# Optimization experiments

Measured on AMD Instinct MI355X. Metric: run time of the kernel, lower is better.

## Reference

```python
import jax, jax.numpy as jnp
import numpy as np


def setup_inputs() -> dict:
    key = jax.random.key(0)
    ks = jax.random.split(key, 10)
    B, S, I, Hy, H = 16, 4096, 256, 64, 512
    sc = 0.05
    return {
        "x": jax.random.normal(ks[0], (B, S, I), jnp.float32),
        "hidden": jax.random.normal(ks[1], (B, H), jnp.float32),
        "lin0_W": jax.random.normal(ks[2], (Hy, I), jnp.float32) * sc,
        "lin0_b": jax.random.normal(ks[3], (Hy,), jnp.float32) * sc,
        "sig0_W": jax.random.normal(ks[4], (Hy, I), jnp.float32) * sc,
        "sig0_b": jax.random.normal(ks[5], (Hy,), jnp.float32) * sc,
        "fch_W": jax.random.normal(ks[6], (H, Hy), jnp.float32) * sc,
        "fch_b": jax.random.normal(ks[7], (H,), jnp.float32) * sc,
        "fc2_W": jax.random.normal(ks[8], (H, I), jnp.float32) * sc,
        "fc2_b": jax.random.normal(ks[9], (H,), jnp.float32) * sc,
    }


def reference(x, hidden, lin0_W, lin0_b, sig0_W, sig0_b, fch_W, fch_b, fc2_W, fc2_b):
    # GLN sub-network (num_layers=1): relu(linear(x) * sigmoid(linear(x)))
    lin = jnp.einsum('bsi,hi->bsh', x, lin0_W) + lin0_b          # [B,S,Hy]
    gate = jax.nn.sigmoid(jnp.einsum('bsi,hi->bsh', x, sig0_W) + sig0_b)
    g = jax.nn.relu(lin * gate)                                   # [B,S,Hy]
    b = jnp.einsum('bsh,dh->bsd', g, fch_W) + fch_b               # [B,S,H]
    # multihead gating
    sig_alphas = jax.nn.sigmoid(jnp.einsum('bsi,di->bsd', x, fc2_W) + fc2_b)
    b = b * sig_alphas

    # sequential recurrence: h_t = relu(b_t + roll(h_{t-1}, 1, -1)); h_{-1} = hidden
    def step(h, b_t):
        h = jax.nn.relu(b_t + jnp.roll(h, 1, axis=-1))
        return h, h

    b_tmajor = jnp.swapaxes(b, 0, 1)  # [S,B,H]
    last, outs = jax.lax.scan(step, hidden, b_tmajor)
    outputs = jnp.swapaxes(outs, 0, 1)  # [B,S,H]
    return outputs, last
```

## Files before the change

kernel.cpp:

```cpp
#include <hip/hip_runtime.h>

typedef __attribute__((ext_vector_type(4))) float  f32x4;
typedef __attribute__((ext_vector_type(4))) short  s16x4;
typedef __attribute__((ext_vector_type(8))) short  s16x8;
typedef __bf16 bf16x8 __attribute__((ext_vector_type(8)));

#define NBATCH 16
#define SEQ    4096
#define KIN    256
#define HY     64
#define HOUT   512
#define NROWS  (NBATCH*SEQ)
#define LC     32
#define NC     (SEQ/LC)

#define GP(x) ((const __attribute__((address_space(1))) void*)(x))
#define LP(x) ((__attribute__((address_space(3))) void*)(x))

static __device__ __forceinline__ short f2bf(float f) {
  unsigned u = __float_as_uint(f);
  u = u + 0x7FFF + ((u >> 16) & 1);
  return (short)(u >> 16);
}
static __device__ __forceinline__ float bf2f(short h) {
  return __uint_as_float(((unsigned)(unsigned short)h) << 16);
}
static __device__ __forceinline__ f32x4 mfma16(bf16x8 a, bf16x8 b, f32x4 c) {
  return __builtin_amdgcn_mfma_f32_16x16x32_bf16(a, b, c, 0, 0, 0);
}
static __device__ __forceinline__ bf16x8 ldfrag(const short* p) {
  return *reinterpret_cast<const bf16x8*>(p);
}
static __device__ __forceinline__ float fsigmoid(float z) {
  return 1.f / (1.f + __expf(-z));
}

__global__ void prep_w(const float* __restrict__ lin0W, const float* __restrict__ sig0W,
                       const float* __restrict__ fchW,  const float* __restrict__ fc2W,
                       short* __restrict__ W1h, short* __restrict__ W2h,
                       short* __restrict__ Fh,  short* __restrict__ F2h) {
  int i = blockIdx.x * 256 + threadIdx.x;
  if (i < 16384) {
    W1h[i] = f2bf(lin0W[i]);
    W2h[i] = f2bf(sig0W[i]);
  } else if (i < 16384 + 32768) {
    Fh[i - 16384] = f2bf(fchW[i - 16384]);
  } else if (i < 16384 + 32768 + 131072) {
    F2h[i - 49152] = f2bf(fc2W[i - 49152]);
  }
}

__global__ __launch_bounds__(256) void gx(
    const float* __restrict__ x,
    const short* __restrict__ W1h, const short* __restrict__ W2h,
    const float* __restrict__ lin0b, const float* __restrict__ sig0b,
    short* __restrict__ Gh, short* __restrict__ xh) {
  __shared__ __align__(16) short smem[64 * 256 + 64 * 64];
  short* Ah = smem;
  short* gL = smem + 64 * 256;
  int tid = threadIdx.x;
  int row0 = blockIdx.x * 64;
  #pragma unroll
  for (int i = 0; i < 8; ++i) {
    int slot = i * 256 + tid;
    int r = slot >> 5, k8 = slot & 31;
    const float* xp = x + (size_t)(row0 + r) * KIN + k8 * 8;
    f32x4 v0 = *reinterpret_cast<const f32x4*>(xp);
    f32x4 v1 = *reinterpret_cast<const f32x4*>(xp + 4);
    s16x8 hh;
    #pragma unroll
    for (int j = 0; j < 4; ++j) { hh[j] = f2bf(v0[j]); hh[4 + j] = f2bf(v1[j]); }
    *reinterpret_cast<s16x8*>(&Ah[(r * 256 + k8 * 8) ^ ((r & 7) << 3)]) = hh;
    *reinterpret_cast<s16x8*>(xh + (size_t)(row0 + r) * KIN + k8 * 8) = hh;
  }
  __syncthreads();
  int w = tid >> 6, l = tid & 63, lr = l & 15, lg = l >> 4;
  {
    int c = w * 16 + lr;
    f32x4 a1[4], a2[4];
    #pragma unroll
    for (int rt = 0; rt < 4; ++rt) { a1[rt] = (f32x4)0.f; a2[rt] = (f32x4)0.f; }
    #pragma unroll
    for (int ks = 0; ks < 8; ++ks) {
      int kk = ks * 32 + lg * 8;
      bf16x8 b1 = ldfrag(W1h + c * 256 + kk);
      bf16x8 b2 = ldfrag(W2h + c * 256 + kk);
      #pragma unroll
      for (int rt = 0; rt < 4; ++rt) {
        int r = rt * 16 + lr;
        bf16x8 a = ldfrag(&Ah[(r * 256 + kk) ^ ((r & 7) << 3)]);
        a1[rt] = mfma16(b1, a, a1[rt]);
        a2[rt] = mfma16(b2, a, a2[rt]);
      }
    }
    f32x4 blv = *reinterpret_cast<const f32x4*>(lin0b + w * 16 + lg * 4);
    f32x4 bsv = *reinterpret_cast<const f32x4*>(sig0b + w * 16 + lg * 4);
    #pragma unroll
    for (int rt = 0; rt < 4; ++rt) {
      int xrl = rt * 16 + lr;
      s16x4 gg;
      #pragma unroll
      for (int j = 0; j < 4; ++j) {
        float g = (a1[rt][j] + blv[j]) * fsigmoid(a2[rt][j] + bsv[j]);
        gg[j] = f2bf(g > 0.f ? g : 0.f);
      }
      *reinterpret_cast<s16x4*>(&gL[(xrl * 64 + w * 16 + lg * 4) ^ ((xrl & 7) << 3)]) = gg;
    }
  }
  __syncthreads();
  #pragma unroll
  for (int i = 0; i < 2; ++i) {
    int slot = i * 256 + tid;
    int row = slot >> 3, c8 = slot & 7;
    s16x8 v = *reinterpret_cast<const s16x8*>(&gL[(row * 64 + c8 * 8) ^ ((row & 7) << 3)]);
    *reinterpret_cast<s16x8*>(Gh + (size_t)(row0 + row) * HY + c8 * 8) = v;
  }
}

__global__ __launch_bounds__(512, 4) void bg(
    const short* __restrict__ xh, const short* __restrict__ Gh,
    const short* __restrict__ F2h, const short* __restrict__ Fh,
    const float* __restrict__ fchb, const float* __restrict__ fc2b,
    short* __restrict__ Bb) {
  __shared__ __align__(16) short smem[2][16384];
  short* bT = &smem[1][0];
  int tid = threadIdx.x;
  int w = tid >> 6, l = tid & 63;
  int lr = l & 15, lg = l >> 4;
  int r0 = (w >> 1) * 32;
  int c0 = (w & 1) * 64;
  int bid = blockIdx.x;
  int xcd = bid & 7, idx = bid >> 3;
  int colTile = xcd >> 1;
  int rowTile = ((xcd & 1) << 8) + idx;
  int row0 = rowTile * 128;
  int col0 = colTile * 128;

  auto stage = [&](int t, int b) {
    short* As = &smem[b][0];
    short* Bs = &smem[b][8192];
    #pragma unroll
    for (int j = 0; j < 2; ++j) {
      int blk = w * 2 + j;
      int flat = blk * 64 + l;
      int row = flat >> 3, sp = flat & 7;
      int seg = sp ^ (row & 7);
      const short* asrc = (t < 4) ? xh + (size_t)(row0 + row) * KIN + t * 64 + seg * 8
                                  : Gh + (size_t)(row0 + row) * HY + seg * 8;
      const short* bsrc = (t < 4) ? F2h + (size_t)(col0 + row) * KIN + t * 64 + seg * 8
                                  : Fh + (size_t)(col0 + row) * HY + seg * 8;
      __builtin_amdgcn_global_load_lds(GP(asrc), LP(&As[blk * 512]), 16, 0, 0);
      __builtin_amdgcn_global_load_lds(GP(bsrc), LP(&Bs[blk * 512]), 16, 0, 0);
    }
  };
  auto compute = [&](int b, f32x4 (&acc)[2][4]) {
    short* As = &smem[b][0];
    short* Bs = &smem[b][8192];
    #pragma unroll
    for (int ksl = 0; ksl < 2; ++ksl) {
      bf16x8 Af[2], Bf[4];
      #pragma unroll
      for (int i = 0; i < 2; ++i) {
        int row = r0 + i * 16 + lr;
        Af[i] = ldfrag(&As[row * 64 + ((ksl * 32 + lg * 8) ^ ((row & 7) << 3))]);
      }
      #pragma unroll
      for (int i = 0; i < 4; ++i) {
        int col = c0 + i * 16 + lr;
        Bf[i] = ldfrag(&Bs[col * 64 + ((ksl * 32 + lg * 8) ^ ((col & 7) << 3))]);
      }
      #pragma unroll
      for (int rt = 0; rt < 2; ++rt)
        #pragma unroll
        for (int ct = 0; ct < 4; ++ct)
          acc[rt][ct] = mfma16(Af[rt], Bf[ct], acc[rt][ct]);
    }
  };

  f32x4 acc2[2][4], accF[2][4];
  #pragma unroll
  for (int rt = 0; rt < 2; ++rt)
    #pragma unroll
    for (int ct = 0; ct < 4; ++ct) { acc2[rt][ct] = (f32x4)0.f; accF[rt][ct] = (f32x4)0.f; }

  stage(0, 0);
  __syncthreads();
  #pragma unroll
  for (int t = 0; t < 4; ++t) {
    stage(t + 1, (t + 1) & 1);
    compute(t & 1, acc2);
    __syncthreads();
  }
  compute(0, accF);

  #pragma unroll
  for (int ct = 0; ct < 4; ++ct) {
    int lc = c0 + ct * 16 + lr;
    int col = col0 + lc;
    float bc = fchb[col], b2c = fc2b[col];
    #pragma unroll
    for (int rt = 0; rt < 2; ++rt) {
      int tl0 = r0 + rt * 16 + lg * 4;
      #pragma unroll
      for (int j = 0; j < 4; ++j) {
        int tl = tl0 + j;
        float alpha = fsigmoid(acc2[rt][ct][j] + b2c);
        bT[(tl * 128 + lc) ^ ((tl & 7) << 3)] = f2bf((accF[rt][ct][j] + bc) * alpha);
      }
    }
  }
  __syncthreads();
  #pragma unroll
  for (int i = 0; i < 4; ++i) {
    int slot = i * 512 + tid;
    int row = slot >> 4, c8 = slot & 15;
    s16x8 vv = *reinterpret_cast<const s16x8*>(&bT[(row * 128 + c8 * 8) ^ ((row & 7) << 3)]);
    *reinterpret_cast<s16x8*>(Bb + (size_t)(row0 + row) * HOUT + col0 + c8 * 8) = vv;
  }
}

__global__ __launch_bounds__(64) void scan_passA(const short* __restrict__ Bb,
                                                 float* __restrict__ Cc, float* __restrict__ Sc) {
  int bc = blockIdx.x;
  int l = threadIdx.x;
  int row0 = bc * LC;
  const short* bp = Bb + (size_t)row0 * HOUT + l * 8;
  s16x8 v0 = *reinterpret_cast<const s16x8*>(bp);
  float C[8], S[8];
  #pragma unroll
  for (int i = 0; i < 8; ++i) { S[i] = bf2f(v0[i]); C[i] = 0.f; }
  s16x8 vc = *reinterpret_cast<const s16x8*>(bp + (size_t)HOUT);
  for (int t = 1; t < LC; ++t) {
    s16x8 vn;
    if (t + 1 < LC) vn = *reinterpret_cast<const s16x8*>(bp + (size_t)(t + 1) * HOUT);
    float bb[8];
    #pragma unroll
    for (int i = 0; i < 8; ++i) bb[i] = bf2f(vc[i]);
    float pC = __shfl(C[7], (l + 63) & 63);
    float pS = __shfl(S[7], (l + 63) & 63);
    #pragma unroll
    for (int i = 7; i >= 1; --i) { C[i] = fmaxf(0.f, bb[i] + C[i - 1]); S[i] = bb[i] + S[i - 1]; }
    C[0] = fmaxf(0.f, bb[0] + pC);
    S[0] = bb[0] + pS;
    vc = vn;
  }
  float* cp = Cc + (size_t)bc * HOUT + l * 8;
  float* sp = Sc + (size_t)bc * HOUT + l * 8;
  #pragma unroll
  for (int i = 0; i < 8; ++i) { cp[i] = C[i]; sp[i] = S[i]; }
}

__global__ __launch_bounds__(64) void scan_combine(const float* __restrict__ hidden,
                                                   const float* __restrict__ Cc, const float* __restrict__ Sc,
                                                   float* __restrict__ hIn, float* __restrict__ lastOut) {
  int batch = blockIdx.x;
  int l = threadIdx.x;
  float h[8];
  const float* hp = hidden + batch * HOUT + l * 8;
  #pragma unroll
  for (int i = 0; i < 8; ++i) h[i] = hp[i];
  size_t base0 = ((size_t)batch * NC) * HOUT + l * 8;
  f32x4 pc0[4], pc1[4], ps0[4], ps1[4];
  #pragma unroll
  for (int s = 0; s < 4; ++s) {
    size_t b = base0 + (size_t)s * HOUT;
    pc0[s] = *reinterpret_cast<const f32x4*>(Cc + b);
    pc1[s] = *reinterpret_cast<const f32x4*>(Cc + b + 4);
    ps0[s] = *reinterpret_cast<const f32x4*>(Sc + b);
    ps1[s] = *reinterpret_cast<const f32x4*>(Sc + b + 4);
  }
  for (int cg = 0; cg < NC; cg += 4) {
    #pragma unroll
    for (int s = 0; s < 4; ++s) {
      int c = cg + s;
      size_t base = base0 + (size_t)c * HOUT;
      f32x4 h0, h1;
      #pragma unroll
      for (int i = 0; i < 4; ++i) { h0[i] = h[i]; h1[i] = h[4 + i]; }
      *reinterpret_cast<f32x4*>(hIn + base) = h0;
      *reinterpret_cast<f32x4*>(hIn + base + 4) = h1;
      float hs[8];
      #pragma unroll
      for (int i = 0; i < 8; ++i) hs[i] = __shfl(h[i], (l + 60) & 63);
      #pragma unroll
      for (int i = 0; i < 4; ++i) {
        h[i]     = fmaxf(pc0[s][i], ps0[s][i] + hs[i]);
        h[4 + i] = fmaxf(pc1[s][i], ps1[s][i] + hs[4 + i]);
      }
      if (c + 4 < NC) {
        size_t nb = base + (size_t)4 * HOUT;
        pc0[s] = *reinterpret_cast<const f32x4*>(Cc + nb);
        pc1[s] = *reinterpret_cast<const f32x4*>(Cc + nb + 4);
        ps0[s] = *reinterpret_cast<const f32x4*>(Sc + nb);
        ps1[s] = *reinterpret_cast<const f32x4*>(Sc + nb + 4);
      }
    }
  }
  float* lp = lastOut + batch * HOUT + l * 8;
  #pragma unroll
  for (int i = 0; i < 8; ++i) lp[i] = h[i];
}

__global__ __launch_bounds__(64) void scan_passB(const short* __restrict__ bws,
                                                 const float* __restrict__ hIn,
                                                 float* __restrict__ hout) {
  int bc = blockIdx.x;
  int l = threadIdx.x;
  int row0 = bc * LC;
  const float* hp = hIn + (size_t)bc * HOUT + l * 8;
  float h[8];
  #pragma unroll
  for (int i = 0; i < 8; ++i) h[i] = hp[i];
  s16x8 vc = *reinterpret_cast<const s16x8*>(bws + (size_t)row0 * HOUT + l * 8);
  for (int t = 0; t < LC; ++t) {
    s16x8 vn;
    if (t + 1 < LC)
      vn = *reinterpret_cast<const s16x8*>(bws + (size_t)(row0 + t + 1) * HOUT + l * 8);
    float bb[8];
    #pragma unroll
    for (int i = 0; i < 8; ++i) bb[i] = bf2f(vc[i]);
    float ph = __shfl(h[7], (l + 63) & 63);
    #pragma unroll
    for (int i = 7; i >= 1; --i) h[i] = fmaxf(0.f, bb[i] + h[i - 1]);
    h[0] = fmaxf(0.f, bb[0] + ph);
    f32x4 o0, o1;
    #pragma unroll
    for (int i = 0; i < 4; ++i) { o0[i] = h[i]; o1[i] = h[4 + i]; }
    float* bt = hout + (size_t)(row0 + t) * HOUT + l * 8;
    *reinterpret_cast<f32x4*>(bt) = o0;
    *reinterpret_cast<f32x4*>(bt + 4) = o1;
    vc = vn;
  }
}

extern "C" void kernel_launch(void* const* d_in, const int* in_sizes, int n_in,
                              void* d_out, int out_size, void* d_ws, size_t ws_size,
                              hipStream_t stream) {
  (void)in_sizes; (void)n_in; (void)out_size; (void)ws_size;
  const float* x      = (const float*)d_in[0];
  const float* hidden = (const float*)d_in[1];
  const float* lin0W  = (const float*)d_in[2];
  const float* lin0b  = (const float*)d_in[3];
  const float* sig0W  = (const float*)d_in[4];
  const float* sig0b  = (const float*)d_in[5];
  const float* fchW   = (const float*)d_in[6];
  const float* fchb   = (const float*)d_in[7];
  const float* fc2W   = (const float*)d_in[8];
  const float* fc2b   = (const float*)d_in[9];
  float* outO  = (float*)d_out;
  float* lastO = outO + (size_t)NROWS * HOUT;

  char* wsb = (char*)d_ws;
  size_t off = 0;
  auto alloc = [&](size_t bytes) { char* p = wsb + off; off += (bytes + 255) & ~(size_t)255; return p; };
  float* Cc  = (float*)alloc((size_t)NBATCH * NC * HOUT * 4);
  float* Sc  = (float*)alloc((size_t)NBATCH * NC * HOUT * 4);
  float* hIn = (float*)alloc((size_t)NBATCH * NC * HOUT * 4);
  short* W1h = (short*)alloc(HY * KIN * 2);
  short* W2h = (short*)alloc(HY * KIN * 2);
  short* Fh  = (short*)alloc(HOUT * HY * 2);
  short* F2h = (short*)alloc(HOUT * KIN * 2);
  short* Gh  = (short*)alloc((size_t)NROWS * HY * 2);
  short* xh  = (short*)alloc((size_t)NROWS * KIN * 2);
  short* Bb  = (short*)alloc((size_t)NROWS * HOUT * 2);

  prep_w<<<704, 256, 0, stream>>>(lin0W, sig0W, fchW, fc2W, W1h, W2h, Fh, F2h);
  gx<<<NROWS / 64, 256, 0, stream>>>(x, W1h, W2h, lin0b, sig0b, Gh, xh);
  bg<<<2048, 512, 0, stream>>>(xh, Gh, F2h, Fh, fchb, fc2b, Bb);
  scan_passA<<<NBATCH * NC, 64, 0, stream>>>(Bb, Cc, Sc);
  scan_combine<<<NBATCH, 64, 0, stream>>>(hidden, Cc, Sc, hIn, lastO);
  scan_passB<<<NBATCH * NC, 64, 0, stream>>>(Bb, hIn, outO);
}
```

Before: 168.3 us.

## Fuse GLN gate GEMM into bg kernel, drop Gh intermediate buffer

The separate gx kernel becomes a plain fp32-to-bf16 conversion of x. The first-layer gated linear projection (lin0/sig0 GEMMs plus sigmoid and relu) now runs inside bg, reusing the x tiles already staged in LDS for the fc2 GEMM. The gate output lands in LDS and feeds the fch GEMM directly, which removes the Gh global write and read. In exchange, each column tile recomputes the gate GEMM (4x redundant work), reads W1/W2 fragments straight from global memory, and carries more accumulator registers. The block-to-tile mapping also changes so the four column tiles of a row tile share an XCD.

```diff
diff --git a/kernel.cpp b/kernel.cpp
--- a/kernel.cpp
+++ b/kernel.cpp
@@ -50,93 +50,38 @@
   }
 }
 
-__global__ __launch_bounds__(256) void gx(
-    const float* __restrict__ x,
+__global__ __launch_bounds__(256) void xcvt(const float* __restrict__ x, short* __restrict__ xh) {
+  size_t i = ((size_t)blockIdx.x * 256 + threadIdx.x) * 8;
+  f32x4 v0 = *reinterpret_cast<const f32x4*>(x + i);
+  f32x4 v1 = *reinterpret_cast<const f32x4*>(x + i + 4);
+  s16x8 hh;
+  #pragma unroll
+  for (int j = 0; j < 4; ++j) { hh[j] = f2bf(v0[j]); hh[4 + j] = f2bf(v1[j]); }
+  *reinterpret_cast<s16x8*>(xh + i) = hh;
+}
+
+__global__ __launch_bounds__(512, 4) void bg(
+    const short* __restrict__ xh,
     const short* __restrict__ W1h, const short* __restrict__ W2h,
+    const short* __restrict__ F2h, const short* __restrict__ Fh,
     const float* __restrict__ lin0b, const float* __restrict__ sig0b,
-    short* __restrict__ Gh, short* __restrict__ xh) {
-  __shared__ __align__(16) short smem[64 * 256 + 64 * 64];
-  short* Ah = smem;
-  short* gL = smem + 64 * 256;
-  int tid = threadIdx.x;
-  int row0 = blockIdx.x * 64;
-  #pragma unroll
-  for (int i = 0; i < 8; ++i) {
-    int slot = i * 256 + tid;
-    int r = slot >> 5, k8 = slot & 31;
-    const float* xp = x + (size_t)(row0 + r) * KIN + k8 * 8;
-    f32x4 v0 = *reinterpret_cast<const f32x4*>(xp);
-    f32x4 v1 = *reinterpret_cast<const f32x4*>(xp + 4);
-    s16x8 hh;
-    #pragma unroll
-    for (int j = 0; j < 4; ++j) { hh[j] = f2bf(v0[j]); hh[4 + j] = f2bf(v1[j]); }
-    *reinterpret_cast<s16x8*>(&Ah[(r * 256 + k8 * 8) ^ ((r & 7) << 3)]) = hh;
-    *reinterpret_cast<s16x8*>(xh + (size_t)(row0 + r) * KIN + k8 * 8) = hh;
-  }
-  __syncthreads();
-  int w = tid >> 6, l = tid & 63, lr = l & 15, lg = l >> 4;
-  {
-    int c = w * 16 + lr;
-    f32x4 a1[4], a2[4];
-    #pragma unroll
-    for (int rt = 0; rt < 4; ++rt) { a1[rt] = (f32x4)0.f; a2[rt] = (f32x4)0.f; }
-    #pragma unroll
-    for (int ks = 0; ks < 8; ++ks) {
-      int kk = ks * 32 + lg * 8;
-      bf16x8 b1 = ldfrag(W1h + c * 256 + kk);
-      bf16x8 b2 = ldfrag(W2h + c * 256 + kk);
-      #pragma unroll
-      for (int rt = 0; rt < 4; ++rt) {
-        int r = rt * 16 + lr;
-        bf16x8 a = ldfrag(&Ah[(r * 256 + kk) ^ ((r & 7) << 3)]);
-        a1[rt] = mfma16(b1, a, a1[rt]);
-        a2[rt] = mfma16(b2, a, a2[rt]);
-      }
-    }
-    f32x4 blv = *reinterpret_cast<const f32x4*>(lin0b + w * 16 + lg * 4);
-    f32x4 bsv = *reinterpret_cast<const f32x4*>(sig0b + w * 16 + lg * 4);
-    #pragma unroll
-    for (int rt = 0; rt < 4; ++rt) {
-      int xrl = rt * 16 + lr;
-      s16x4 gg;
-      #pragma unroll
-      for (int j = 0; j < 4; ++j) {
-        float g = (a1[rt][j] + blv[j]) * fsigmoid(a2[rt][j] + bsv[j]);
-        gg[j] = f2bf(g > 0.f ? g : 0.f);
-      }
-      *reinterpret_cast<s16x4*>(&gL[(xrl * 64 + w * 16 + lg * 4) ^ ((xrl & 7) << 3)]) = gg;
-    }
-  }
-  __syncthreads();
-  #pragma unroll
-  for (int i = 0; i < 2; ++i) {
-    int slot = i * 256 + tid;
-    int row = slot >> 3, c8 = slot & 7;
-    s16x8 v = *reinterpret_cast<const s16x8*>(&gL[(row * 64 + c8 * 8) ^ ((row & 7) << 3)]);
-    *reinterpret_cast<s16x8*>(Gh + (size_t)(row0 + row) * HY + c8 * 8) = v;
-  }
-}
-
-__global__ __launch_bounds__(512, 4) void bg(
-    const short* __restrict__ xh, const short* __restrict__ Gh,
-    const short* __restrict__ F2h, const short* __restrict__ Fh,
     const float* __restrict__ fchb, const float* __restrict__ fc2b,
     short* __restrict__ Bb) {
   __shared__ __align__(16) short smem[2][16384];
-  short* bT = &smem[1][0];
   int tid = threadIdx.x;
   int w = tid >> 6, l = tid & 63;
   int lr = l & 15, lg = l >> 4;
   int r0 = (w >> 1) * 32;
   int c0 = (w & 1) * 64;
+  int hy0 = (w & 1) * 32;
   int bid = blockIdx.x;
   int xcd = bid & 7, idx = bid >> 3;
-  int colTile = xcd >> 1;
-  int rowTile = ((xcd & 1) << 8) + idx;
+  int rowTile = (xcd << 6) + (idx >> 2);
+  int colTile = idx & 3;
   int row0 = rowTile * 128;
   int col0 = colTile * 128;
 
-  auto stage = [&](int t, int b) {
+  auto stageAB = [&](int t, int b) {
     short* As = &smem[b][0];
     short* Bs = &smem[b][8192];
     #pragma unroll
@@ -145,54 +90,128 @@
       int flat = blk * 64 + l;
       int row = flat >> 3, sp = flat & 7;
       int seg = sp ^ (row & 7);
-      const short* asrc = (t < 4) ? xh + (size_t)(row0 + row) * KIN + t * 64 + seg * 8
-                                  : Gh + (size_t)(row0 + row) * HY + seg * 8;
-      const short* bsrc = (t < 4) ? F2h + (size_t)(col0 + row) * KIN + t * 64 + seg * 8
-                                  : Fh + (size_t)(col0 + row) * HY + seg * 8;
+      const short* asrc = xh + (size_t)(row0 + row) * KIN + t * 64 + seg * 8;
+      const short* bsrc = F2h + (size_t)(col0 + row) * KIN + t * 64 + seg * 8;
       __builtin_amdgcn_global_load_lds(GP(asrc), LP(&As[blk * 512]), 16, 0, 0);
       __builtin_amdgcn_global_load_lds(GP(bsrc), LP(&Bs[blk * 512]), 16, 0, 0);
     }
   };
-  auto compute = [&](int b, f32x4 (&acc)[2][4]) {
+  auto stageB4 = [&](int b) {
+    short* Bs = &smem[b][8192];
+    #pragma unroll
+    for (int j = 0; j < 2; ++j) {
+      int blk = w * 2 + j;
+      int flat = blk * 64 + l;
+      int row = flat >> 3, sp = flat & 7;
+      int seg = sp ^ (row & 7);
+      const short* bsrc = Fh + (size_t)(col0 + row) * HY + seg * 8;
+      __builtin_amdgcn_global_load_lds(GP(bsrc), LP(&Bs[blk * 512]), 16, 0, 0);
+    }
+  };
+
+  f32x4 acc2[2][4], accg1[2][2], accg2[2][2];
+  #pragma unroll
+  for (int rt = 0; rt < 2; ++rt) {
+    #pragma unroll
+    for (int ct = 0; ct < 4; ++ct) acc2[rt][ct] = (f32x4)0.f;
+    #pragma unroll
+    for (int wt = 0; wt < 2; ++wt) { accg1[wt][rt] = (f32x4)0.f; accg2[wt][rt] = (f32x4)0.f; }
+  }
+
+  auto computeM = [&](int b, int kbase) {
     short* As = &smem[b][0];
     short* Bs = &smem[b][8192];
     #pragma unroll
     for (int ksl = 0; ksl < 2; ++ksl) {
-      bf16x8 Af[2], Bf[4];
+      int kk = ksl * 32 + lg * 8;
+      bf16x8 Af[2], Bf[4], W1f[2], W2f[2];
       #pragma unroll
       for (int i = 0; i < 2; ++i) {
         int row = r0 + i * 16 + lr;
-        Af[i] = ldfrag(&As[row * 64 + ((ksl * 32 + lg * 8) ^ ((row & 7) << 3))]);
+        Af[i] = ldfrag(&As[row * 64 + (kk ^ ((row & 7) << 3))]);
       }
       #pragma unroll
       for (int i = 0; i < 4; ++i) {
         int col = c0 + i * 16 + lr;
-        Bf[i] = ldfrag(&Bs[col * 64 + ((ksl * 32 + lg * 8) ^ ((col & 7) << 3))]);
+        Bf[i] = ldfrag(&Bs[col * 64 + (kk ^ ((col & 7) << 3))]);
+      }
+      #pragma unroll
+      for (int i = 0; i < 2; ++i) {
+        int hy = hy0 + i * 16 + lr;
+        W1f[i] = ldfrag(W1h + hy * 256 + kbase + kk);
+        W2f[i] = ldfrag(W2h + hy * 256 + kbase + kk);
+      }
+      #pragma unroll
+      for (int rt = 0; rt < 2; ++rt) {
+        #pragma unroll
+        for (int ct = 0; ct < 4; ++ct)
+          acc2[rt][ct] = mfma16(Af[rt], Bf[ct], acc2[rt][ct]);
+        #pragma unroll
+        for (int wt = 0; wt < 2; ++wt) {
+          accg1[wt][rt] = mfma16(W1f[wt], Af[rt], accg1[wt][rt]);
+          accg2[wt][rt] = mfma16(W2f[wt], Af[rt], accg2[wt][rt]);
+        }
+      }
+    }
+  };
+
+  stageAB(0, 0);
+  __syncthreads();
+  #pragma unroll
+  for (int t = 0; t < 4; ++t) {
+    if (t < 3) stageAB(t + 1, (t + 1) & 1);
+    else       stageB4(0);
+    computeM(t & 1, t * 64);
+    __syncthreads();
+  }
+  short* gL = &smem[1][0];
+  #pragma unroll
+  for (int wt = 0; wt < 2; ++wt) {
+    f32x4 blv = *reinterpret_cast<const f32x4*>(lin0b + hy0 + wt * 16 + lg * 4);
+    f32x4 bsv = *reinterpret_cast<const f32x4*>(sig0b + hy0 + wt * 16 + lg * 4);
+    #pragma unroll
+    for (int rt = 0; rt < 2; ++rt) {
+      int xrl = r0 + rt * 16 + lr;
+      s16x4 gg;
+      #pragma unroll
+      for (int j = 0; j < 4; ++j) {
+        float g = (accg1[wt][rt][j] + blv[j]) * fsigmoid(accg2[wt][rt][j] + bsv[j]);
+        gg[j] = f2bf(g > 0.f ? g : 0.f);
+      }
+      *reinterpret_cast<s16x4*>(&gL[(xrl * 64 + hy0 + wt * 16 + lg * 4) ^ ((xrl & 7) << 3)]) = gg;
+    }
+  }
+  __syncthreads();
+  f32x4 accF[2][4];
+  #pragma unroll
+  for (int rt = 0; rt < 2; ++rt)
+    #pragma unroll
+    for (int ct = 0; ct < 4; ++ct) accF[rt][ct] = (f32x4)0.f;
+  {
+    short* Bs = &smem[0][8192];
+    #pragma unroll
+    for (int ksl = 0; ksl < 2; ++ksl) {
+      int kk = ksl * 32 + lg * 8;
+      bf16x8 Af[2], Bf[4];
+      #pragma unroll
+      for (int i = 0; i < 2; ++i) {
+        int row = r0 + i * 16 + lr;
+        Af[i] = ldfrag(&gL[row * 64 + (kk ^ ((row & 7) << 3))]);
+      }
+      #pragma unroll
+      for (int i = 0; i < 4; ++i) {
+        int col = c0 + i * 16 + lr;
+        Bf[i] = ldfrag(&Bs[col * 64 + (kk ^ ((col & 7) << 3))]);
       }
       #pragma unroll
       for (int rt = 0; rt < 2; ++rt)
         #pragma unroll
         for (int ct = 0; ct < 4; ++ct)
-          acc[rt][ct] = mfma16(Af[rt], Bf[ct], acc[rt][ct]);
-    }
-  };
-
-  f32x4 acc2[2][4], accF[2][4];
-  #pragma unroll
-  for (int rt = 0; rt < 2; ++rt)
-    #pragma unroll
-    for (int ct = 0; ct < 4; ++ct) { acc2[rt][ct] = (f32x4)0.f; accF[rt][ct] = (f32x4)0.f; }
-
-  stage(0, 0);
+          accF[rt][ct] = mfma16(Af[rt], Bf[ct], accF[rt][ct]);
+    }
+  }
   __syncthreads();
-  #pragma unroll
-  for (int t = 0; t < 4; ++t) {
-    stage(t + 1, (t + 1) & 1);
-    compute(t & 1, acc2);
-    __syncthreads();
-  }
-  compute(0, accF);
-
+  short* bT = &smem[0][0];
   #pragma unroll
   for (int ct = 0; ct < 4; ++ct) {
     int lc = c0 + ct * 16 + lr;
@@ -360,13 +379,12 @@
   short* W2h = (short*)alloc(HY * KIN * 2);
   short* Fh  = (short*)alloc(HOUT * HY * 2);
   short* F2h = (short*)alloc(HOUT * KIN * 2);
-  short* Gh  = (short*)alloc((size_t)NROWS * HY * 2);
   short* xh  = (short*)alloc((size_t)NROWS * KIN * 2);
   short* Bb  = (short*)alloc((size_t)NROWS * HOUT * 2);
 
   prep_w<<<704, 256, 0, stream>>>(lin0W, sig0W, fchW, fc2W, W1h, W2h, Fh, F2h);
-  gx<<<NROWS / 64, 256, 0, stream>>>(x, W1h, W2h, lin0b, sig0b, Gh, xh);
-  bg<<<2048, 512, 0, stream>>>(xh, Gh, F2h, Fh, fchb, fc2b, Bb);
+  xcvt<<<NROWS * KIN / 8 / 256, 256, 0, stream>>>(x, xh);
+  bg<<<2048, 512, 0, stream>>>(xh, W1h, W2h, F2h, Fh, lin0b, sig0b, fchb, fc2b, Bb);
   scan_passA<<<NBATCH * NC, 64, 0, stream>>>(Bb, Cc, Sc);
   scan_combine<<<NBATCH, 64, 0, stream>>>(hidden, Cc, Sc, hIn, lastO);
   scan_passB<<<NBATCH * NC, 64, 0, stream>>>(Bb, hIn, outO);
```

Result: slower. 220.8 us (+31.2%).
